# Kernel optimization log

Measured on AMD Instinct MI355X. Metric: run time of the kernel, lower is better.

The kernel has to match this reference:

```python
import jax, jax.numpy as jnp
import numpy as np

MODEL_DIM = 128
N_ATOMS = 2048
ATOM_SIZE = 512
N_SAMPLES = 2 ** 15
FACTOR = 1.0
TAU = 1.0
B, E = 8, 64


def _stack(x, w0, b0, w1, b1, w2, b2):
    # LinearOutputStack(model_dim, 2, out_channels=...): 2 hidden layers + output
    h = jax.nn.leaky_relu(x @ w0 + b0, 0.2)
    h = jax.nn.leaky_relu(h @ w1 + b1, 0.2)
    return h @ w2 + b2


def _fft_shift(a, shift):
    # a: [B, E, n], shift: [B, E, 1] (fractional shift in units of n samples * 0.5)
    n = a.shape[-1]
    shift_samples = shift * n * 0.5  # [B, E, 1]
    a = jnp.pad(a, ((0, 0), (0, 0), (0, n * 2)))
    spec = jnp.fft.rfft(a, axis=-1, norm='ortho')  # [B, E, n_coeffs] complex
    n_coeffs = spec.shape[-1]
    phase = (jnp.arange(n_coeffs) * 2j * jnp.pi) / n_coeffs  # [n_coeffs]
    spec = spec * jnp.exp(-phase[None, None, :] * shift_samples)
    samples = jnp.fft.irfft(spec, axis=-1, norm='ortho')
    return samples[..., :n]


def setup_inputs() -> dict:
    key = jax.random.key(0)
    ks = jax.random.split(key, 24)
    w = lambda k, i, o: (jax.random.normal(k, (i, o), jnp.float32) * 0.1)
    z = lambda o: jnp.zeros((o,), jnp.float32)
    return {
        'x': jax.random.normal(ks[0], (B, E, MODEL_DIM), jnp.float32),
        'times': jax.random.uniform(ks[1], (B, E, 1), jnp.float32),
        'gumbel_u': jax.random.uniform(ks[2], (B, E, N_ATOMS), jnp.float32),
        'atoms': jax.random.uniform(ks[3], (N_ATOMS, ATOM_SIZE), jnp.float32, -1.0, 1.0),
        'tw0': w(ks[4], MODEL_DIM, MODEL_DIM), 'tb0': z(MODEL_DIM),
        'tw1': w(ks[5], MODEL_DIM, MODEL_DIM), 'tb1': z(MODEL_DIM),
        'tw2': w(ks[6], MODEL_DIM, 1), 'tb2': z(1),
        'sw0': w(ks[7], MODEL_DIM, MODEL_DIM), 'sb0': z(MODEL_DIM),
        'sw1': w(ks[8], MODEL_DIM, MODEL_DIM), 'sb1': z(MODEL_DIM),
        'sw2': w(ks[9], MODEL_DIM, N_ATOMS), 'sb2': z(N_ATOMS),
        'aw0': w(ks[10], MODEL_DIM, MODEL_DIM), 'ab0': z(MODEL_DIM),
        'aw1': w(ks[11], MODEL_DIM, MODEL_DIM), 'ab1': z(MODEL_DIM),
        'aw2': w(ks[12], MODEL_DIM, 1), 'ab2': z(1),
    }


def reference(x, times, gumbel_u, atoms,
              tw0, tb0, tw1, tb1, tw2, tb2,
              sw0, sb0, sw1, sb1, sw2, sb2,
              aw0, ab0, aw1, ab1, aw2, ab2):
    time = jax.nn.sigmoid(_stack(x, tw0, tb0, tw1, tb1, tw2, tb2)) * FACTOR + times  # [B,E,1]
    amp = _stack(x, aw0, ab0, aw1, ab1, aw2, ab2) ** 2  # [B,E,1]
    logits = _stack(x, sw0, sb0, sw1, sb1, sw2, sb2)  # [B,E,N_ATOMS]

    # hard gumbel-softmax with straight-through estimator
    eps = 1e-10
    g = -jnp.log(-jnp.log(gumbel_u + eps) + eps)
    y_soft = jax.nn.softmax((logits + g) / TAU, axis=-1)
    y_hard = jax.nn.one_hot(jnp.argmax(y_soft, axis=-1), N_ATOMS, dtype=y_soft.dtype)
    sel = y_hard - jax.lax.stop_gradient(y_soft) + y_soft

    normed = atoms / (jnp.linalg.norm(atoms, axis=-1, keepdims=True) + 1e-8)
    a = (sel @ normed) * amp  # [B,E,ATOM_SIZE]
    a = jnp.pad(a, ((0, 0), (0, 0), (0, N_SAMPLES - ATOM_SIZE)))  # [B,E,N_SAMPLES]
    final = _fft_shift(a, time)
    return jnp.sum(final, axis=1, keepdims=True)  # [B,1,N_SAMPLES]
```

## Files before the change

### kernel.cpp

```cpp
#include <hip/hip_runtime.h>
#include <math.h>

#define MD 128
#define NA 2048
#define AS 512
#define NS 32768
#define NBE 512
#define W1 768
#define W2 1280
#define PI 3.14159265358979323846
#define KTH ((float)(PI / 98304.0))

__device__ __forceinline__ float lrelu(float v) { return v > 0.f ? v : 0.2f * v; }

__device__ __forceinline__ float p8_far(float tf, float4 A, float4 B, float4 C)
{
  float u  = tf - A.x;
  float th = u * KTH;
  float sn = __sinf(th);
  float cs = __cosf(th);
  float c  = cs * __builtin_amdgcn_rcpf(sn);
  float u2  = __builtin_fmaf(c, c, 1.f);
  float c2  = c + c;
  float u22 = u2 + u2;
  float a2  = c * u2;
  float a3  = (-1.f / 3.f) * __builtin_fmaf(c2, a2, u2 * u2);
  float a4  = 0.5f * __builtin_fmaf(-c, a3, u2 * a2);
  float s5  = __builtin_fmaf(c2, a4, a2 * a2);
  s5        = __builtin_fmaf(-u22, a3, s5);
  float a5  = -0.2f * s5;
  float s6  = __builtin_fmaf(c, a5, a2 * a3);
  s6        = __builtin_fmaf(-u2, a4, s6);
  float a6  = (-1.f / 3.f) * s6;
  float s7  = __builtin_fmaf(c2, a6, a3 * a3);
  s7        = __builtin_fmaf(-u22, a5, s7);
  s7        = __builtin_fmaf(2.f * a2, a4, s7);
  float a7  = (-1.f / 7.f) * s7;
  float s8  = __builtin_fmaf(c, a7, a3 * a4);
  s8        = __builtin_fmaf(-u2, a6, s8);
  s8        = __builtin_fmaf(a2, a5, s8);
  float a8  = -0.25f * s8;
  float y = c * A.w;
  y = __builtin_fmaf(-u2, B.x, y);
  y = __builtin_fmaf(a2, B.y, y);
  y = __builtin_fmaf(a3, B.z, y);
  y = __builtin_fmaf(a4, B.w, y);
  y = __builtin_fmaf(a5, C.x, y);
  y = __builtin_fmaf(a6, C.y, y);
  y = __builtin_fmaf(a7, C.z, y);
  y = __builtin_fmaf(a8, C.w, y);
  bool farq = (tf < A.y) || (tf >= A.z);
  return farq ? y : 0.f;
}

__global__ __launch_bounds__(128) void hidden_kernel(
    const float* __restrict__ x, const float* __restrict__ times,
    const float* __restrict__ tw0, const float* __restrict__ tb0,
    const float* __restrict__ tw1, const float* __restrict__ tb1,
    const float* __restrict__ tw2, const float* __restrict__ tb2,
    const float* __restrict__ sw0, const float* __restrict__ sb0,
    const float* __restrict__ sw1, const float* __restrict__ sb1,
    const float* __restrict__ aw0, const float* __restrict__ ab0,
    const float* __restrict__ aw1, const float* __restrict__ ab1,
    const float* __restrict__ aw2, const float* __restrict__ ab2,
    float* __restrict__ timev, float* __restrict__ ampv,
    float* __restrict__ h2sel)
{
  const int rg = blockIdx.x;
  const int stack = blockIdx.y;
  const int tid = threadIdx.x;

  __shared__ float xs[4][MD];
  __shared__ double dA[4][MD], dB[4][MD];
  __shared__ float fA[4][MD], fB[4][MD];

#pragma unroll
  for (int j = 0; j < 4; ++j) xs[j][tid] = x[(rg * 4 + j) * MD + tid];
  __syncthreads();

  if (stack == 0) {
    {
      double b = (double)tb0[tid];
      double s[4] = {b, b, b, b};
#pragma unroll 8
      for (int k = 0; k < MD; ++k) {
        double w = (double)tw0[k * MD + tid];
#pragma unroll
        for (int j = 0; j < 4; ++j) s[j] += (double)xs[j][k] * w;
      }
#pragma unroll
      for (int j = 0; j < 4; ++j) dA[j][tid] = s[j] > 0.0 ? s[j] : 0.2 * s[j];
      __syncthreads();
    }
    {
      double b = (double)tb1[tid];
      double s[4] = {b, b, b, b};
#pragma unroll 8
      for (int k = 0; k < MD; ++k) {
        double w = (double)tw1[k * MD + tid];
#pragma unroll
        for (int j = 0; j < 4; ++j) s[j] += dA[j][k] * w;
      }
#pragma unroll
      for (int j = 0; j < 4; ++j) dB[j][tid] = s[j] > 0.0 ? s[j] : 0.2 * s[j];
      __syncthreads();
    }
    {
      double w2 = (double)tw2[tid];
#pragma unroll
      for (int j = 0; j < 4; ++j) dA[j][tid] = dB[j][tid] * w2;
      __syncthreads();
      for (int off = 64; off > 0; off >>= 1) {
        if (tid < off) {
#pragma unroll
          for (int j = 0; j < 4; ++j) dA[j][tid] += dA[j][tid + off];
        }
        __syncthreads();
      }
      if (tid == 0) {
#pragma unroll
        for (int j = 0; j < 4; ++j) {
          double tval = dA[j][0] + (double)tb2[0];
          double sg = 1.0 / (1.0 + exp(-tval));
          float tf = (float)sg;
          timev[rg * 4 + j] = tf * 1.0f + times[rg * 4 + j];
        }
      }
    }
  } else if (stack == 1) {
    {
      float b = ab0[tid];
      float s[4] = {b, b, b, b};
#pragma unroll 8
      for (int k = 0; k < MD; ++k) {
        float w = aw0[k * MD + tid];
#pragma unroll
        for (int j = 0; j < 4; ++j) s[j] += xs[j][k] * w;
      }
#pragma unroll
      for (int j = 0; j < 4; ++j) fA[j][tid] = lrelu(s[j]);
      __syncthreads();
    }
    {
      float b = ab1[tid];
      float s[4] = {b, b, b, b};
#pragma unroll 8
      for (int k = 0; k < MD; ++k) {
        float w = aw1[k * MD + tid];
#pragma unroll
        for (int j = 0; j < 4; ++j) s[j] += fA[j][k] * w;
      }
#pragma unroll
      for (int j = 0; j < 4; ++j) fB[j][tid] = lrelu(s[j]);
      __syncthreads();
    }
    {
      float w2 = aw2[tid];
#pragma unroll
      for (int j = 0; j < 4; ++j) fA[j][tid] = fB[j][tid] * w2;
      __syncthreads();
      for (int off = 64; off > 0; off >>= 1) {
        if (tid < off) {
#pragma unroll
          for (int j = 0; j < 4; ++j) fA[j][tid] += fA[j][tid + off];
        }
        __syncthreads();
      }
      if (tid == 0) {
#pragma unroll
        for (int j = 0; j < 4; ++j) {
          float av = fA[j][0] + ab2[0];
          ampv[rg * 4 + j] = av * av;
        }
      }
    }
  } else {
    {
      float b = sb0[tid];
      float s[4] = {b, b, b, b};
#pragma unroll 8
      for (int k = 0; k < MD; ++k) {
        float w = sw0[k * MD + tid];
#pragma unroll
        for (int j = 0; j < 4; ++j) s[j] += xs[j][k] * w;
      }
#pragma unroll
      for (int j = 0; j < 4; ++j) fA[j][tid] = lrelu(s[j]);
      __syncthreads();
    }
    {
      float b = sb1[tid];
      float s[4] = {b, b, b, b};
#pragma unroll 8
      for (int k = 0; k < MD; ++k) {
        float w = sw1[k * MD + tid];
#pragma unroll
        for (int j = 0; j < 4; ++j) s[j] += fA[j][k] * w;
      }
#pragma unroll
      for (int j = 0; j < 4; ++j)
        h2sel[(rg * 4 + j) * MD + tid] = lrelu(s[j]);
    }
  }
}

__global__ __launch_bounds__(128) void logits_kernel(
    const float* __restrict__ h2sel, const float* __restrict__ gu,
    const float* __restrict__ sw2, const float* __restrict__ sb2,
    float2* __restrict__ partials)
{
  const int ot = blockIdx.x;
  const int beg = blockIdx.y;
  const int tid = threadIdx.x;
  const int o = ot * 128 + tid;
  const int wave = tid >> 6, lane = tid & 63;

  __shared__ float h2s[4][MD];
  __shared__ float wv[2][4];
  __shared__ int wi[2][4];

#pragma unroll
  for (int j = 0; j < 4; ++j) h2s[j][tid] = h2sel[(beg * 4 + j) * MD + tid];
  __syncthreads();

  float b = sb2[o];
  float acc[4] = {b, b, b, b};
#pragma unroll 16
  for (int k = 0; k < MD; ++k) {
    float w = sw2[k * NA + o];
#pragma unroll
    for (int j = 0; j < 4; ++j) acc[j] = fmaf(h2s[j][k], w, acc[j]);
  }

#pragma unroll
  for (int j = 0; j < 4; ++j) {
    float u = gu[(beg * 4 + j) * NA + o];
    float g = -logf(-logf(u + 1e-10f) + 1e-10f);
    float v = acc[j] + g;
    int idx = o;
    for (int off = 32; off > 0; off >>= 1) {
      float ov = __shfl_xor(v, off);
      int oi = __shfl_xor(idx, off);
      if (ov > v || (ov == v && oi < idx)) { v = ov; idx = oi; }
    }
    if (lane == 0) { wv[wave][j] = v; wi[wave][j] = idx; }
  }
  __syncthreads();
  if (tid == 0) {
#pragma unroll
    for (int j = 0; j < 4; ++j) {
      float v0 = wv[0][j], v1 = wv[1][j];
      int i0 = wi[0][j], i1 = wi[1][j];
      bool take1 = (v1 > v0) || (v1 == v0 && i1 < i0);
      float bv = take1 ? v1 : v0;
      int bi = take1 ? i1 : i0;
      partials[(beg * 4 + j) * 16 + ot] = make_float2(bv, __int_as_float(bi));
    }
  }
}

__global__ __launch_bounds__(128) void finalize_kernel(
    const float2* __restrict__ partials, const float* __restrict__ timev,
    const float* __restrict__ ampv, const float* __restrict__ atoms,
    float* __restrict__ G, int* __restrict__ m0s, float* __restrict__ fracs,
    float4* __restrict__ params, float4* __restrict__ mom2)
{
  const int be = blockIdx.x;
  const int tid = threadIdx.x;
  __shared__ float red[128];
  __shared__ float m_red[128][13];
  __shared__ float sc_coef, sc_inv;
  __shared__ int sc_idx;

  if (tid < 64) {
    float v = -3.4e38f;
    int idx = 0x7fffffff;
    if (tid < 16) {
      float2 p = partials[be * 16 + tid];
      v = p.x;
      idx = __float_as_int(p.y);
    }
    for (int off = 8; off > 0; off >>= 1) {
      float ov = __shfl_xor(v, off);
      int oi = __shfl_xor(idx, off);
      if (ov > v || (ov == v && oi < idx)) { v = ov; idx = oi; }
    }
    if (tid == 0) sc_idx = idx;
  }
  __syncthreads();
  const int idx = sc_idx;

  {
    float ss = 0.f;
    for (int i = tid; i < AS; i += 128) { float v = atoms[idx * AS + i]; ss += v * v; }
    red[tid] = ss;
    __syncthreads();
    for (int off = 64; off > 0; off >>= 1) {
      if (tid < off) red[tid] += red[tid + off];
      __syncthreads();
    }
    if (tid == 0) {
      sc_inv = 1.f / (sqrtf(red[0]) + 1e-8f);
      double Nc = (double)timev[be] * (1610612736.0 / 49153.0);
      double rr = rint(Nc);
      int m0 = (int)rr;
      float fr = (float)(Nc - rr);
      if (fabsf(fr) < 1e-9f) fr = (fr < 0.f) ? -1e-9f : 1e-9f;
      m0s[be] = m0;
      fracs[be] = fr;
      sc_coef = ampv[be] * ((m0 & 1) ? 1.0f : -1.0f) *
                sinf((float)PI * fr) * (1.0f / 98304.0f);
      red[64] = (float)m0;
      red[65] = fr;
    }
    __syncthreads();
  }

  const float cf = sc_coef * sc_inv;
  float mk[13];
#pragma unroll
  for (int k = 0; k < 13; ++k) mk[k] = 0.f;
  for (int t = tid; t < AS; t += 128) {
    float av = atoms[idx * AS + t] * cf;
    float gv = (t & 1) ? -av : av;
    G[be * AS + t] = gv;
    float q = (255.5f - (float)t) * KTH;
    float pw = gv;
    mk[0] += pw;
#pragma unroll
    for (int k = 1; k < 13; ++k) { pw *= q; mk[k] += pw; }
  }
#pragma unroll
  for (int k = 0; k < 13; ++k) m_red[tid][k] = mk[k];
  __syncthreads();
  for (int off = 64; off > 0; off >>= 1) {
    if (tid < off) {
#pragma unroll
      for (int k = 0; k < 13; ++k) m_red[tid][k] += m_red[tid + off][k];
    }
    __syncthreads();
  }
  if (tid == 0) {
    int m0 = (int)red[64];
    float fr = red[65];
    float uc = (float)((double)m0 + (double)fr + 255.5);
    params[be * 3 + 0] = make_float4(uc, (float)(m0 - W1), (float)(m0 + W2), m_red[0][0]);
    params[be * 3 + 1] = make_float4(m_red[0][1], m_red[0][2], m_red[0][3], m_red[0][4]);
    params[be * 3 + 2] = make_float4(m_red[0][5], m_red[0][6], m_red[0][7], m_red[0][8]);
    mom2[be] = make_float4(m_red[0][9], m_red[0][10], m_red[0][11], m_red[0][12]);
  }
}

__global__ __launch_bounds__(64) void coeff_kernel(
    const float4* __restrict__ params, const float4* __restrict__ mom2,
    float* __restrict__ Bcoef, int* __restrict__ scount,
    int* __restrict__ slist)
{
  const int tile = blockIdx.x;
  const int bi   = blockIdx.y;
  const int e    = threadIdx.x;
  const int be   = bi * 64 + e;

  const float4 A  = params[be * 3 + 0];
  const float4 B4 = params[be * 3 + 1];
  const float4 C4 = params[be * 3 + 2];
  const float4 D4 = mom2[be];
  const float M[13] = {A.w, B4.x, B4.y, B4.z, B4.w,
                       C4.x, C4.y, C4.z, C4.w, D4.x, D4.y, D4.z, D4.w};

  const float ts = (float)(tile * 128);
  const float te = ts + 128.f;
  const float lo = A.y, hi = A.z;
  const bool inter   = (lo < te) && (hi > ts);
  const bool inside  = (lo <= ts) && (te <= hi);
  const bool special = inter && !inside;

  float Bj[13];
#pragma unroll
  for (int j = 0; j < 13; ++j) Bj[j] = 0.f;

  if (!inter) {
    const float th = (ts + 63.5f - A.x) * KTH;
    const float sn = __sinf(th), cs = __cosf(th);
    const float c = cs * __builtin_amdgcn_rcpf(sn);
    float a[13];
    a[0] = c; a[1] = -__builtin_fmaf(c, c, 1.f);
    float s;
    s = 2.f * a[0] * a[1];                                      a[2]  = -0.5f * s;
    s = __builtin_fmaf(2.f * a[0], a[2], a[1] * a[1]);          a[3]  = (-1.f / 3.f) * s;
    s = 2.f * (a[0] * a[3] + a[1] * a[2]);                      a[4]  = -0.25f * s;
    s = __builtin_fmaf(2.f, a[0] * a[4] + a[1] * a[3], a[2] * a[2]); a[5] = -0.2f * s;
    s = 2.f * (a[0] * a[5] + a[1] * a[4] + a[2] * a[3]);        a[6]  = (-1.f / 6.f) * s;
    s = __builtin_fmaf(2.f, a[0] * a[6] + a[1] * a[5] + a[2] * a[4], a[3] * a[3]); a[7] = (-1.f / 7.f) * s;
    s = 2.f * (a[0] * a[7] + a[1] * a[6] + a[2] * a[5] + a[3] * a[4]); a[8] = -0.125f * s;
    s = __builtin_fmaf(2.f, a[0] * a[8] + a[1] * a[7] + a[2] * a[6] + a[3] * a[5], a[4] * a[4]); a[9] = (-1.f / 9.f) * s;
    s = 2.f * (a[0] * a[9] + a[1] * a[8] + a[2] * a[7] + a[3] * a[6] + a[4] * a[5]); a[10] = -0.1f * s;
    s = __builtin_fmaf(2.f, a[0] * a[10] + a[1] * a[9] + a[2] * a[8] + a[3] * a[7] + a[4] * a[6], a[5] * a[5]); a[11] = (-1.f / 11.f) * s;
    s = 2.f * (a[0] * a[11] + a[1] * a[10] + a[2] * a[9] + a[3] * a[8] + a[4] * a[7] + a[5] * a[6]); a[12] = (-1.f / 12.f) * s;

    const float BIN[13][13] = {
      {1,0,0,0,0,0,0,0,0,0,0,0,0},
      {1,1,0,0,0,0,0,0,0,0,0,0,0},
      {1,2,1,0,0,0,0,0,0,0,0,0,0},
      {1,3,3,1,0,0,0,0,0,0,0,0,0},
      {1,4,6,4,1,0,0,0,0,0,0,0,0},
      {1,5,10,10,5,1,0,0,0,0,0,0,0},
      {1,6,15,20,15,6,1,0,0,0,0,0,0},
      {1,7,21,35,35,21,7,1,0,0,0,0,0},
      {1,8,28,56,70,56,28,8,1,0,0,0,0},
      {1,9,36,84,126,126,84,36,9,1,0,0,0},
      {1,10,45,120,210,252,210,120,45,10,1,0,0},
      {1,11,55,165,330,462,462,330,165,55,11,1,0},
      {1,12,66,220,495,792,924,792,495,220,66,12,1}};
#pragma unroll
    for (int j = 0; j < 13; ++j) {
      float acc = 0.f;
#pragma unroll
      for (int m = j; m < 13; ++m)
        acc = __builtin_fmaf(BIN[m][j] * a[m], M[m - j], acc);
      Bj[j] = acc;
    }
  }

#pragma unroll
  for (int j = 0; j < 13; ++j) {
#pragma unroll
    for (int off = 32; off > 0; off >>= 1)
      Bj[j] += __shfl_xor(Bj[j], off);
  }
  if (e == 0) {
    const int base = (bi * 256 + tile) * 16;
#pragma unroll
    for (int j = 0; j < 13; ++j) Bcoef[base + j] = Bj[j];
  }

  unsigned long long msk = __ballot(special);
  if (special) {
    int pos = __popcll(msk & ((1ull << e) - 1ull));
    slist[(bi * 256 + tile) * 64 + pos] = be;
  }
  if (e == 0) scount[bi * 256 + tile] = (int)__popcll(msk);
}

__global__ __launch_bounds__(256) void field_kernel(
    const float4* __restrict__ params, const float* __restrict__ G,
    const int* __restrict__ m0s, const float* __restrict__ fracs,
    const float* __restrict__ Bcoef, const int* __restrict__ scount,
    const int* __restrict__ slist, float* __restrict__ out)
{
  __shared__ float4 SMEM[768];
  const int bid = blockIdx.x;
  const int tid = threadIdx.x;

  if (bid >= 512) {
    const int idx2 = bid - 512;
    const int b = idx2 >> 7;
    const int seg = idx2 & 127;
    const int t = seg * 256 + tid;
    int tile = __builtin_amdgcn_readfirstlane(t >> 7);
    const int cbase = ((b << 8) + tile) << 4;
    const float c0 = Bcoef[cbase + 0],  c1 = Bcoef[cbase + 1];
    const float c2 = Bcoef[cbase + 2],  c3 = Bcoef[cbase + 3];
    const float c4 = Bcoef[cbase + 4],  c5 = Bcoef[cbase + 5];
    const float c6 = Bcoef[cbase + 6],  c7 = Bcoef[cbase + 7];
    const float c8 = Bcoef[cbase + 8],  c9 = Bcoef[cbase + 9];
    const float c10 = Bcoef[cbase + 10], c11 = Bcoef[cbase + 11];
    const float c12 = Bcoef[cbase + 12];
    const float tf = (float)t;
    const float h = (tf - ((float)(tile * 128) + 63.5f)) * KTH;
    float y = c12;
    y = __builtin_fmaf(y, h, c11);
    y = __builtin_fmaf(y, h, c10);
    y = __builtin_fmaf(y, h, c9);
    y = __builtin_fmaf(y, h, c8);
    y = __builtin_fmaf(y, h, c7);
    y = __builtin_fmaf(y, h, c6);
    y = __builtin_fmaf(y, h, c5);
    y = __builtin_fmaf(y, h, c4);
    y = __builtin_fmaf(y, h, c3);
    y = __builtin_fmaf(y, h, c2);
    y = __builtin_fmaf(y, h, c1);
    y = __builtin_fmaf(y, h, c0);

    const int cnt = __builtin_amdgcn_readfirstlane(scount[(b << 8) + tile]);
    for (int i = 0; i < cnt; ++i) {
      const int se = slist[((b << 8) + tile) * 64 + i];
      const float4 A  = params[se * 3 + 0];
      const float4 B4 = params[se * 3 + 1];
      const float4 C4 = params[se * 3 + 2];
      y += p8_far(tf, A, B4, C4);
    }
    atomicAdd(&out[b * NS + t], (t & 1) ? -y : y);
    return;
  }

  const int be = bid;
  const int m0 = m0s[be];
  const int start = m0 - W1;
  if (start >= NS) return;
  const float fr = fracs[be];
  const int b = be >> 6;

  float4* Tsplit = SMEM;
  float*  Tf = (float*)Tsplit;
  float*  Gl = (float*)(SMEM + 640);
  const float4* Gl4 = SMEM + 640;

  for (int i = tid; i < AS; i += 256) Gl[i] = G[be * AS + i];
  for (int i = tid; i < 2560; i += 256) {
    int v = start - 511 + i;
    float w = (float)(v - m0) - fr;
    float th = w * KTH;
    float q = th * th;
    float sn = th * __builtin_fmaf(q, __builtin_fmaf(q, (1.f / 120.f), (-1.f / 6.f)), 1.f);
    float cs = __builtin_fmaf(q, __builtin_fmaf(q, (1.f / 24.f), -0.5f), 1.f);
    float val = cs * __builtin_amdgcn_rcpf(sn);
    int g = i >> 2;
    int s = (g >> 1) * 4 + (i & 3) + (g & 1) * 1280;
    Tf[s] = val;
  }
  __syncthreads();

  float acc[8];
#pragma unroll
  for (int r = 0; r < 8; ++r) acc[r] = 0.f;

  float Wf[16];
  {
    float4 qa = Tsplit[tid];
    float4 qb = Tsplit[320 + tid];
    Wf[0] = qa.x; Wf[1] = qa.y; Wf[2] = qa.z; Wf[3] = qa.w;
    Wf[4] = qb.x; Wf[5] = qb.y; Wf[6] = qb.z; Wf[7] = qb.w;
  }
#pragma unroll 4
  for (int k = 0; k < 64; ++k) {
    float4 qa = Tsplit[tid + k + 1];
    float4 qb = Tsplit[320 + tid + k + 1];
    Wf[8]  = qa.x; Wf[9]  = qa.y; Wf[10] = qa.z; Wf[11] = qa.w;
    Wf[12] = qb.x; Wf[13] = qb.y; Wf[14] = qb.z; Wf[15] = qb.w;
    const int tc = 504 - 8 * k;
    const float4 gq0 = Gl4[tc >> 2];
    const float4 gq1 = Gl4[(tc >> 2) + 1];
    const float gvals[8] = {gq0.x, gq0.y, gq0.z, gq0.w,
                            gq1.x, gq1.y, gq1.z, gq1.w};
#pragma unroll
    for (int d = 0; d < 8; ++d) {
      const float gv = gvals[d];
#pragma unroll
      for (int r = 0; r < 8; ++r)
        acc[r] = fmaf(gv, Wf[7 + r - d], acc[r]);
    }
#pragma unroll
    for (int m = 0; m < 8; ++m) Wf[m] = Wf[m + 8];
  }

  const int tb = start + tid * 8;
#pragma unroll
  for (int r = 0; r < 8; ++r) {
    int t = tb + r;
    if (t >= 0 && t < NS) {
      float v = (t & 1) ? -acc[r] : acc[r];
      atomicAdd(&out[b * NS + t], v);
    }
  }
}

extern "C" void kernel_launch(void* const* d_in, const int* in_sizes, int n_in,
                              void* d_out, int out_size, void* d_ws, size_t ws_size,
                              hipStream_t stream) {
  const float* x     = (const float*)d_in[0];
  const float* times = (const float*)d_in[1];
  const float* gu    = (const float*)d_in[2];
  const float* atoms = (const float*)d_in[3];
  const float* tw0 = (const float*)d_in[4];  const float* tb0 = (const float*)d_in[5];
  const float* tw1 = (const float*)d_in[6];  const float* tb1 = (const float*)d_in[7];
  const float* tw2 = (const float*)d_in[8];  const float* tb2 = (const float*)d_in[9];
  const float* sw0 = (const float*)d_in[10]; const float* sb0 = (const float*)d_in[11];
  const float* sw1 = (const float*)d_in[12]; const float* sb1 = (const float*)d_in[13];
  const float* sw2 = (const float*)d_in[14]; const float* sb2 = (const float*)d_in[15];
  const float* aw0 = (const float*)d_in[16]; const float* ab0 = (const float*)d_in[17];
  const float* aw1 = (const float*)d_in[18]; const float* ab1 = (const float*)d_in[19];
  const float* aw2 = (const float*)d_in[20]; const float* ab2 = (const float*)d_in[21];

  char* wsb = (char*)d_ws;
  float*  G        = (float*)wsb;
  int*    m0s      = (int*)(wsb + 1048576);
  float*  fracs    = (float*)(wsb + 1050624);
  float4* params   = (float4*)(wsb + 1052672);
  float*  timev    = (float*)(wsb + 1077248);
  float*  ampv     = (float*)(wsb + 1079296);
  float4* mom2     = (float4*)(wsb + 1081344);
  float*  h2sel    = (float*)(wsb + 1089536);
  float2* partials = (float2*)(wsb + 1351680);
  float*  Bcoef    = (float*)(wsb + 1089536);
  int*    scount   = (int*)(wsb + 1220608);
  int*    slist    = (int*)(wsb + 1228800);

  hipMemsetAsync(d_out, 0, (size_t)out_size * sizeof(float), stream);

  hidden_kernel<<<dim3(NBE / 4, 3), 128, 0, stream>>>(
      x, times, tw0, tb0, tw1, tb1, tw2, tb2,
      sw0, sb0, sw1, sb1, aw0, ab0, aw1, ab1, aw2, ab2,
      timev, ampv, h2sel);

  logits_kernel<<<dim3(16, NBE / 4), 128, 0, stream>>>(h2sel, gu, sw2, sb2, partials);

  finalize_kernel<<<NBE, 128, 0, stream>>>(partials, timev, ampv, atoms,
                                           G, m0s, fracs, params, mom2);

  coeff_kernel<<<dim3(256, 8), 64, 0, stream>>>(params, mom2, Bcoef, scount, slist);

  field_kernel<<<1536, 256, 0, stream>>>(params, G, m0s, fracs,
                                         Bcoef, scount, slist, (float*)d_out);
}
```

Before: 76.17 us.

## Fuse coeff kernel into field kernel and fold output zeroing into hidden kernel

Removes the separate coeff_kernel launch by computing per-tile polynomial coefficients and special-event lists inside each field_kernel block's first two wavefronts, sharing them through shared memory. Replaces hipMemsetAsync with a grid-stride zero store inside hidden_kernel, and vectorizes the atom reads and G stores in finalize_kernel with float4. This cuts two launches and the global round-trip of Bcoef/slist. In exchange each field block redoes the coefficient work for its tiles, and the other waves wait on a barrier.

After: 69.27 us. 9.1% less time.

```diff
diff --git a/kernel.cpp b/kernel.cpp
--- a/kernel.cpp
+++ b/kernel.cpp
@@ -64,11 +64,18 @@
     const float* __restrict__ aw1, const float* __restrict__ ab1,
     const float* __restrict__ aw2, const float* __restrict__ ab2,
     float* __restrict__ timev, float* __restrict__ ampv,
-    float* __restrict__ h2sel)
+    float* __restrict__ h2sel, float* __restrict__ out)
 {
   const int rg = blockIdx.x;
   const int stack = blockIdx.y;
   const int tid = threadIdx.x;
+
+  {
+    const int gtid = (stack * 128 + rg) * 128 + tid;
+    float4* out4 = (float4*)out;
+    const float4 z = make_float4(0.f, 0.f, 0.f, 0.f);
+    for (int i = gtid; i < (8 * NS) / 4; i += 49152) out4[i] = z;
+  }
 
   __shared__ float xs[4][MD];
   __shared__ double dA[4][MD], dB[4][MD];
@@ -290,9 +297,10 @@
   __syncthreads();
   const int idx = sc_idx;
 
+  const float4 a4 = ((const float4*)(atoms + (size_t)idx * AS))[tid];
+
   {
-    float ss = 0.f;
-    for (int i = tid; i < AS; i += 128) { float v = atoms[idx * AS + i]; ss += v * v; }
+    float ss = a4.x * a4.x + a4.y * a4.y + a4.z * a4.z + a4.w * a4.w;
     red[tid] = ss;
     __syncthreads();
     for (int off = 64; off > 0; off >>= 1) {
@@ -320,16 +328,22 @@
   float mk[13];
 #pragma unroll
   for (int k = 0; k < 13; ++k) mk[k] = 0.f;
-  for (int t = tid; t < AS; t += 128) {
-    float av = atoms[idx * AS + t] * cf;
-    float gv = (t & 1) ? -av : av;
-    G[be * AS + t] = gv;
+  const float av4[4] = {a4.x * cf, a4.y * cf, a4.z * cf, a4.w * cf};
+  float4 gv4;
+  float* gvp = (float*)&gv4;
+  const int t0 = tid * 4;
+#pragma unroll
+  for (int j = 0; j < 4; ++j) {
+    const int t = t0 + j;
+    float gv = (j & 1) ? -av4[j] : av4[j];
+    gvp[j] = gv;
     float q = (255.5f - (float)t) * KTH;
     float pw = gv;
     mk[0] += pw;
 #pragma unroll
     for (int k = 1; k < 13; ++k) { pw *= q; mk[k] += pw; }
   }
+  ((float4*)(G + (size_t)be * AS))[tid] = gv4;
 #pragma unroll
   for (int k = 0; k < 13; ++k) m_red[tid][k] = mk[k];
   __syncthreads();
@@ -351,102 +365,10 @@
   }
 }
 
-__global__ __launch_bounds__(64) void coeff_kernel(
+__global__ __launch_bounds__(256) void field_kernel(
     const float4* __restrict__ params, const float4* __restrict__ mom2,
-    float* __restrict__ Bcoef, int* __restrict__ scount,
-    int* __restrict__ slist)
-{
-  const int tile = blockIdx.x;
-  const int bi   = blockIdx.y;
-  const int e    = threadIdx.x;
-  const int be   = bi * 64 + e;
-
-  const float4 A  = params[be * 3 + 0];
-  const float4 B4 = params[be * 3 + 1];
-  const float4 C4 = params[be * 3 + 2];
-  const float4 D4 = mom2[be];
-  const float M[13] = {A.w, B4.x, B4.y, B4.z, B4.w,
-                       C4.x, C4.y, C4.z, C4.w, D4.x, D4.y, D4.z, D4.w};
-
-  const float ts = (float)(tile * 128);
-  const float te = ts + 128.f;
-  const float lo = A.y, hi = A.z;
-  const bool inter   = (lo < te) && (hi > ts);
-  const bool inside  = (lo <= ts) && (te <= hi);
-  const bool special = inter && !inside;
-
-  float Bj[13];
-#pragma unroll
-  for (int j = 0; j < 13; ++j) Bj[j] = 0.f;
-
-  if (!inter) {
-    const float th = (ts + 63.5f - A.x) * KTH;
-    const float sn = __sinf(th), cs = __cosf(th);
-    const float c = cs * __builtin_amdgcn_rcpf(sn);
-    float a[13];
-    a[0] = c; a[1] = -__builtin_fmaf(c, c, 1.f);
-    float s;
-    s = 2.f * a[0] * a[1];                                      a[2]  = -0.5f * s;
-    s = __builtin_fmaf(2.f * a[0], a[2], a[1] * a[1]);          a[3]  = (-1.f / 3.f) * s;
-    s = 2.f * (a[0] * a[3] + a[1] * a[2]);                      a[4]  = -0.25f * s;
-    s = __builtin_fmaf(2.f, a[0] * a[4] + a[1] * a[3], a[2] * a[2]); a[5] = -0.2f * s;
-    s = 2.f * (a[0] * a[5] + a[1] * a[4] + a[2] * a[3]);        a[6]  = (-1.f / 6.f) * s;
-    s = __builtin_fmaf(2.f, a[0] * a[6] + a[1] * a[5] + a[2] * a[4], a[3] * a[3]); a[7] = (-1.f / 7.f) * s;
-    s = 2.f * (a[0] * a[7] + a[1] * a[6] + a[2] * a[5] + a[3] * a[4]); a[8] = -0.125f * s;
-    s = __builtin_fmaf(2.f, a[0] * a[8] + a[1] * a[7] + a[2] * a[6] + a[3] * a[5], a[4] * a[4]); a[9] = (-1.f / 9.f) * s;
-    s = 2.f * (a[0] * a[9] + a[1] * a[8] + a[2] * a[7] + a[3] * a[6] + a[4] * a[5]); a[10] = -0.1f * s;
-    s = __builtin_fmaf(2.f, a[0] * a[10] + a[1] * a[9] + a[2] * a[8] + a[3] * a[7] + a[4] * a[6], a[5] * a[5]); a[11] = (-1.f / 11.f) * s;
-    s = 2.f * (a[0] * a[11] + a[1] * a[10] + a[2] * a[9] + a[3] * a[8] + a[4] * a[7] + a[5] * a[6]); a[12] = (-1.f / 12.f) * s;
-
-    const float BIN[13][13] = {
-      {1,0,0,0,0,0,0,0,0,0,0,0,0},
-      {1,1,0,0,0,0,0,0,0,0,0,0,0},
-      {1,2,1,0,0,0,0,0,0,0,0,0,0},
-      {1,3,3,1,0,0,0,0,0,0,0,0,0},
-      {1,4,6,4,1,0,0,0,0,0,0,0,0},
-      {1,5,10,10,5,1,0,0,0,0,0,0,0},
-      {1,6,15,20,15,6,1,0,0,0,0,0,0},
-      {1,7,21,35,35,21,7,1,0,0,0,0,0},
-      {1,8,28,56,70,56,28,8,1,0,0,0,0},
-      {1,9,36,84,126,126,84,36,9,1,0,0,0},
-      {1,10,45,120,210,252,210,120,45,10,1,0,0},
-      {1,11,55,165,330,462,462,330,165,55,11,1,0},
-      {1,12,66,220,495,792,924,792,495,220,66,12,1}};
-#pragma unroll
-    for (int j = 0; j < 13; ++j) {
-      float acc = 0.f;
-#pragma unroll
-      for (int m = j; m < 13; ++m)
-        acc = __builtin_fmaf(BIN[m][j] * a[m], M[m - j], acc);
-      Bj[j] = acc;
-    }
-  }
-
-#pragma unroll
-  for (int j = 0; j < 13; ++j) {
-#pragma unroll
-    for (int off = 32; off > 0; off >>= 1)
-      Bj[j] += __shfl_xor(Bj[j], off);
-  }
-  if (e == 0) {
-    const int base = (bi * 256 + tile) * 16;
-#pragma unroll
-    for (int j = 0; j < 13; ++j) Bcoef[base + j] = Bj[j];
-  }
-
-  unsigned long long msk = __ballot(special);
-  if (special) {
-    int pos = __popcll(msk & ((1ull << e) - 1ull));
-    slist[(bi * 256 + tile) * 64 + pos] = be;
-  }
-  if (e == 0) scount[bi * 256 + tile] = (int)__popcll(msk);
-}
-
-__global__ __launch_bounds__(256) void field_kernel(
-    const float4* __restrict__ params, const float* __restrict__ G,
-    const int* __restrict__ m0s, const float* __restrict__ fracs,
-    const float* __restrict__ Bcoef, const int* __restrict__ scount,
-    const int* __restrict__ slist, float* __restrict__ out)
+    const float* __restrict__ G, const int* __restrict__ m0s,
+    const float* __restrict__ fracs, float* __restrict__ out)
 {
   __shared__ float4 SMEM[768];
   const int bid = blockIdx.x;
@@ -456,35 +378,117 @@
     const int idx2 = bid - 512;
     const int b = idx2 >> 7;
     const int seg = idx2 & 127;
+    float* Cf   = (float*)SMEM;
+    int*   scnt = (int*)(Cf + 32);
+    int*   slst = scnt + 2;
+
+    const int w = tid >> 6;
+    const int e = tid & 63;
+    if (w < 2) {
+      const int tile = 2 * seg + w;
+      const int be = b * 64 + e;
+      const float4 A  = params[be * 3 + 0];
+      const float4 B4 = params[be * 3 + 1];
+      const float4 C4 = params[be * 3 + 2];
+      const float4 D4 = mom2[be];
+      const float M[13] = {A.w, B4.x, B4.y, B4.z, B4.w,
+                           C4.x, C4.y, C4.z, C4.w, D4.x, D4.y, D4.z, D4.w};
+
+      const float ts = (float)(tile * 128);
+      const float te = ts + 128.f;
+      const float lo = A.y, hi = A.z;
+      const bool inter   = (lo < te) && (hi > ts);
+      const bool inside  = (lo <= ts) && (te <= hi);
+      const bool special = inter && !inside;
+
+      float Bj[13];
+#pragma unroll
+      for (int j = 0; j < 13; ++j) Bj[j] = 0.f;
+
+      if (!inter) {
+        const float th = (ts + 63.5f - A.x) * KTH;
+        const float sn = __sinf(th), cs = __cosf(th);
+        const float c = cs * __builtin_amdgcn_rcpf(sn);
+        float a[13];
+        a[0] = c; a[1] = -__builtin_fmaf(c, c, 1.f);
+        float s;
+        s = 2.f * a[0] * a[1];                                      a[2]  = -0.5f * s;
+        s = __builtin_fmaf(2.f * a[0], a[2], a[1] * a[1]);          a[3]  = (-1.f / 3.f) * s;
+        s = 2.f * (a[0] * a[3] + a[1] * a[2]);                      a[4]  = -0.25f * s;
+        s = __builtin_fmaf(2.f, a[0] * a[4] + a[1] * a[3], a[2] * a[2]); a[5] = -0.2f * s;
+        s = 2.f * (a[0] * a[5] + a[1] * a[4] + a[2] * a[3]);        a[6]  = (-1.f / 6.f) * s;
+        s = __builtin_fmaf(2.f, a[0] * a[6] + a[1] * a[5] + a[2] * a[4], a[3] * a[3]); a[7] = (-1.f / 7.f) * s;
+        s = 2.f * (a[0] * a[7] + a[1] * a[6] + a[2] * a[5] + a[3] * a[4]); a[8] = -0.125f * s;
+        s = __builtin_fmaf(2.f, a[0] * a[8] + a[1] * a[7] + a[2] * a[6] + a[3] * a[5], a[4] * a[4]); a[9] = (-1.f / 9.f) * s;
+        s = 2.f * (a[0] * a[9] + a[1] * a[8] + a[2] * a[7] + a[3] * a[6] + a[4] * a[5]); a[10] = -0.1f * s;
+        s = __builtin_fmaf(2.f, a[0] * a[10] + a[1] * a[9] + a[2] * a[8] + a[3] * a[7] + a[4] * a[6], a[5] * a[5]); a[11] = (-1.f / 11.f) * s;
+        s = 2.f * (a[0] * a[11] + a[1] * a[10] + a[2] * a[9] + a[3] * a[8] + a[4] * a[7] + a[5] * a[6]); a[12] = (-1.f / 12.f) * s;
+
+        const float BIN[13][13] = {
+          {1,0,0,0,0,0,0,0,0,0,0,0,0},
+          {1,1,0,0,0,0,0,0,0,0,0,0,0},
+          {1,2,1,0,0,0,0,0,0,0,0,0,0},
+          {1,3,3,1,0,0,0,0,0,0,0,0,0},
+          {1,4,6,4,1,0,0,0,0,0,0,0,0},
+          {1,5,10,10,5,1,0,0,0,0,0,0,0},
+          {1,6,15,20,15,6,1,0,0,0,0,0,0},
+          {1,7,21,35,35,21,7,1,0,0,0,0,0},
+          {1,8,28,56,70,56,28,8,1,0,0,0,0},
+          {1,9,36,84,126,126,84,36,9,1,0,0,0},
+          {1,10,45,120,210,252,210,120,45,10,1,0,0},
+          {1,11,55,165,330,462,462,330,165,55,11,1,0},
+          {1,12,66,220,495,792,924,792,495,220,66,12,1}};
+#pragma unroll
+        for (int j = 0; j < 13; ++j) {
+          float acc = 0.f;
+#pragma unroll
+          for (int m = j; m < 13; ++m)
+            acc = __builtin_fmaf(BIN[m][j] * a[m], M[m - j], acc);
+          Bj[j] = acc;
+        }
+      }
+
+#pragma unroll
+      for (int j = 0; j < 13; ++j) {
+#pragma unroll
+        for (int off = 32; off > 0; off >>= 1)
+          Bj[j] += __shfl_xor(Bj[j], off);
+      }
+      if (e == 0) {
+#pragma unroll
+        for (int j = 0; j < 13; ++j) Cf[w * 16 + j] = Bj[j];
+      }
+      unsigned long long msk = __ballot(special);
+      if (special) {
+        int pos = __popcll(msk & ((1ull << e) - 1ull));
+        slst[w * 64 + pos] = be;
+      }
+      if (e == 0) scnt[w] = (int)__popcll(msk);
+    }
+    __syncthreads();
+
     const int t = seg * 256 + tid;
-    int tile = __builtin_amdgcn_readfirstlane(t >> 7);
-    const int cbase = ((b << 8) + tile) << 4;
-    const float c0 = Bcoef[cbase + 0],  c1 = Bcoef[cbase + 1];
-    const float c2 = Bcoef[cbase + 2],  c3 = Bcoef[cbase + 3];
-    const float c4 = Bcoef[cbase + 4],  c5 = Bcoef[cbase + 5];
-    const float c6 = Bcoef[cbase + 6],  c7 = Bcoef[cbase + 7];
-    const float c8 = Bcoef[cbase + 8],  c9 = Bcoef[cbase + 9];
-    const float c10 = Bcoef[cbase + 10], c11 = Bcoef[cbase + 11];
-    const float c12 = Bcoef[cbase + 12];
+    const int tw = tid >> 7;
+    const float* cc = Cf + tw * 16;
     const float tf = (float)t;
-    const float h = (tf - ((float)(tile * 128) + 63.5f)) * KTH;
-    float y = c12;
-    y = __builtin_fmaf(y, h, c11);
-    y = __builtin_fmaf(y, h, c10);
-    y = __builtin_fmaf(y, h, c9);
-    y = __builtin_fmaf(y, h, c8);
-    y = __builtin_fmaf(y, h, c7);
-    y = __builtin_fmaf(y, h, c6);
-    y = __builtin_fmaf(y, h, c5);
-    y = __builtin_fmaf(y, h, c4);
-    y = __builtin_fmaf(y, h, c3);
-    y = __builtin_fmaf(y, h, c2);
-    y = __builtin_fmaf(y, h, c1);
-    y = __builtin_fmaf(y, h, c0);
-
-    const int cnt = __builtin_amdgcn_readfirstlane(scount[(b << 8) + tile]);
+    const float h = (tf - ((float)((2 * seg + tw) * 128) + 63.5f)) * KTH;
+    float y = cc[12];
+    y = __builtin_fmaf(y, h, cc[11]);
+    y = __builtin_fmaf(y, h, cc[10]);
+    y = __builtin_fmaf(y, h, cc[9]);
+    y = __builtin_fmaf(y, h, cc[8]);
+    y = __builtin_fmaf(y, h, cc[7]);
+    y = __builtin_fmaf(y, h, cc[6]);
+    y = __builtin_fmaf(y, h, cc[5]);
+    y = __builtin_fmaf(y, h, cc[4]);
+    y = __builtin_fmaf(y, h, cc[3]);
+    y = __builtin_fmaf(y, h, cc[2]);
+    y = __builtin_fmaf(y, h, cc[1]);
+    y = __builtin_fmaf(y, h, cc[0]);
+
+    const int cnt = scnt[tw];
     for (int i = 0; i < cnt; ++i) {
-      const int se = slist[((b << 8) + tile) * 64 + i];
+      const int se = slst[tw * 64 + i];
       const float4 A  = params[se * 3 + 0];
       const float4 B4 = params[se * 3 + 1];
       const float4 C4 = params[se * 3 + 2];
@@ -592,24 +596,17 @@
   float4* mom2     = (float4*)(wsb + 1081344);
   float*  h2sel    = (float*)(wsb + 1089536);
   float2* partials = (float2*)(wsb + 1351680);
-  float*  Bcoef    = (float*)(wsb + 1089536);
-  int*    scount   = (int*)(wsb + 1220608);
-  int*    slist    = (int*)(wsb + 1228800);
-
-  hipMemsetAsync(d_out, 0, (size_t)out_size * sizeof(float), stream);
 
   hidden_kernel<<<dim3(NBE / 4, 3), 128, 0, stream>>>(
       x, times, tw0, tb0, tw1, tb1, tw2, tb2,
       sw0, sb0, sw1, sb1, aw0, ab0, aw1, ab1, aw2, ab2,
-      timev, ampv, h2sel);
+      timev, ampv, h2sel, (float*)d_out);
 
   logits_kernel<<<dim3(16, NBE / 4), 128, 0, stream>>>(h2sel, gu, sw2, sb2, partials);
 
   finalize_kernel<<<NBE, 128, 0, stream>>>(partials, timev, ampv, atoms,
                                            G, m0s, fracs, params, mom2);
 
-  coeff_kernel<<<dim3(256, 8), 64, 0, stream>>>(params, mom2, Bcoef, scount, slist);
-
-  field_kernel<<<1536, 256, 0, stream>>>(params, G, m0s, fracs,
-                                         Bcoef, scount, slist, (float*)d_out);
+  field_kernel<<<1536, 256, 0, stream>>>(params, mom2, G, m0s, fracs,
+                                         (float*)d_out);
 }
```
